# Performance work log

Measured on AMD Instinct MI355X. Metric: run time of the kernel, lower is better.

## Reference

```python
import jax, jax.numpy as jnp
import numpy as np


def setup_inputs() -> dict:
    key = jax.random.key(0)
    k1, k2 = jax.random.split(key)
    x = jax.random.normal(k1, (32, 112, 112, 64), dtype=jnp.float32)
    kernels = jax.random.normal(k2, (3, 3, 64, 128), dtype=jnp.float32) * 0.05
    biases = jnp.zeros((128,), dtype=jnp.float32)
    return {"x": x, "kernels": kernels, "biases": biases}


def reference(x, kernels, biases):
    # Stride-1 VALID cross-correlation, NHWC input, HWIO kernel -> NHWC output.
    # Matches the original's per-pixel sum(patch * kernel) over all input channels.
    out = jax.lax.conv_general_dilated(
        x, kernels,
        window_strides=(1, 1),
        padding="VALID",
        dimension_numbers=("NHWC", "HWIO", "NHWC"),
    )
    out = out + biases  # broadcast over (B, H_out, W_out, F)
    return jax.nn.relu(out)  # activation=relu per init_kwargs
```

## Files before the change

kernel.cpp:

```cpp
#include <hip/hip_runtime.h>
#include <hip/hip_bf16.h>

typedef __attribute__((ext_vector_type(4))) float f32x4;
typedef __attribute__((ext_vector_type(8))) short bf16x8;
typedef __attribute__((ext_vector_type(8))) unsigned short u16x8;
typedef __attribute__((ext_vector_type(4))) unsigned int u32x4;

#define HH 112
#define WW 112
#define CIN 64
#define COUT 128
#define HOUT 110
#define WOUT 110
#define MTOT 387200
#define NWG 3025
#define NXCD 8
#define XNE 25690112

__device__ __forceinline__ unsigned short f2bf(float f) {
  unsigned int x = __float_as_uint(f);
  x += 0x7fffu + ((x >> 16) & 1u);
  return (unsigned short)(x >> 16);
}

__device__ __forceinline__ unsigned int cvt2(float lo, float hi) {
  union { __hip_bfloat162 h; unsigned int u; } cv;
  cv.h = __float22bfloat162_rn(float2{lo, hi});
  return cv.u;
}

__device__ __forceinline__ void gload16(const unsigned short* g, unsigned short* l) {
  __builtin_amdgcn_global_load_lds(
      (const __attribute__((address_space(1))) void*)g,
      (__attribute__((address_space(3))) void*)l, 16, 0, 0);
}

__global__ __launch_bounds__(256)
void cvt_x_kernel(const float* __restrict__ x, unsigned short* __restrict__ xb) {
  const int t = blockIdx.x * 256 + threadIdx.x;
  const f32x4* s = (const f32x4*)x + (size_t)t * 2;
  f32x4 a = s[0], b = s[1];
  u32x4 v;
  v[0] = cvt2(a[0], a[1]); v[1] = cvt2(a[2], a[3]);
  v[2] = cvt2(b[0], b[1]); v[3] = cvt2(b[2], b[3]);
  ((u32x4*)xb)[t] = v;
}

__global__ void prepack_b_kernel(const float* __restrict__ kern,
                                 unsigned short* __restrict__ bt) {
  int idx = blockIdx.x * 256 + threadIdx.x;
  if (idx >= 9 * 8192) return;
  int tap = idx >> 13;
  int rem = idx & 8191;
  int co = rem >> 6;
  int e = rem & 63;
  int ci = ((e * 2) ^ ((co & 7) << 4)) >> 1;
  bt[idx] = f2bf(kern[(tap * 64 + ci) * COUT + co]);
}

__global__ __launch_bounds__(512, 4)
void conv_dma_kernel(const unsigned short* __restrict__ xb,
                     const unsigned short* __restrict__ bt,
                     const float* __restrict__ bias,
                     float* __restrict__ out) {
  __shared__ __align__(16) unsigned short As[3][8192];
  __shared__ __align__(16) unsigned short Bs[2][8192];

  const int tid = threadIdx.x;
  const int lane = tid & 63;
  const int wid = tid >> 6;

  const int bid = blockIdx.x;
  const int q = NWG / NXCD, r = NWG % NXCD;
  const int xcd = bid % NXCD, i8 = bid / NXCD;
  const int wg = (xcd < r ? xcd * (q + 1) : r * (q + 1) + (xcd - r) * q) + i8;
  const int m0 = wg * 128;

  int aoff[2];
  const int obase = wid * 2048 + lane * 16;
#pragma unroll
  for (int j = 0; j < 2; ++j) {
    const int o = obase + j * 1024;
    const int rr = o >> 7;
    const int sp = ((o >> 4) & 7) ^ (rr & 7);
    const int m = m0 + rr;
    const int wo = m % WOUT;
    const int t1 = m / WOUT;
    const int ho = t1 % HOUT;
    const int bb = t1 / HOUT;
    aoff[j] = (((bb * HH) + ho) * WW + wo) * CIN + sp * 8;
  }
  const int ldsw0 = wid * 1024;
  const int ldsw1 = wid * 1024 + 512;
  const int blin0 = ldsw0 + lane * 8;
  const int blin1 = ldsw1 + lane * 8;

  const int wm = wid >> 1;
  const int wn = wid & 1;
  const int l16 = lane & 15;
  const int lk = lane >> 4;
  const int swzR = (l16 & 7) << 4;

  const int aroff0 = (wm * 32 + 0 + l16) * 64;
  const int aroff1 = (wm * 32 + 16 + l16) * 64;
  const int broff0 = (wn * 64 + 0 + l16) * 64;
  const int broff1 = (wn * 64 + 16 + l16) * 64;
  const int broff2 = (wn * 64 + 32 + l16) * 64;
  const int broff3 = (wn * 64 + 48 + l16) * 64;

  f32x4 acc[2][4];
#pragma unroll
  for (int i = 0; i < 2; ++i)
#pragma unroll
    for (int j = 0; j < 4; ++j)
      acc[i][j] = (f32x4){0.f, 0.f, 0.f, 0.f};

  auto tapoff = [](int tap) {
    const int kh = tap / 3;
    const int kw = tap - kh * 3;
    return (kh * WW + kw) * CIN;
  };

  gload16(bt + blin0, &Bs[0][ldsw0]);
  gload16(bt + blin1, &Bs[0][ldsw1]);
  gload16(xb + aoff[0], &As[0][ldsw0]);
  gload16(xb + aoff[1], &As[0][ldsw1]);
  {
    const int te = tapoff(1);
    gload16(xb + aoff[0] + te, &As[1][ldsw0]);
    gload16(xb + aoff[1] + te, &As[1][ldsw1]);
  }

#pragma unroll
  for (int kk = 0; kk < 9; ++kk) {
    if (kk < 8) {
      asm volatile("s_waitcnt vmcnt(2)" ::: "memory");
    } else {
      asm volatile("s_waitcnt vmcnt(0)" ::: "memory");
    }
    __builtin_amdgcn_s_barrier();

    if (kk < 8) {
      const int tb = (kk + 1) * 8192;
      unsigned short* bd = Bs[(kk + 1) & 1];
      gload16(bt + tb + blin0, bd + ldsw0);
      gload16(bt + tb + blin1, bd + ldsw1);
    }
    if (kk < 7) {
      const int te = tapoff(kk + 2);
      unsigned short* ad = As[(kk + 2) % 3];
      gload16(xb + aoff[0] + te, ad + ldsw0);
      gload16(xb + aoff[1] + te, ad + ldsw1);
    }

    const unsigned short* Ac = As[kk % 3];
    const unsigned short* Bc = Bs[kk & 1];
#pragma unroll
    for (int ks = 0; ks < 2; ++ks) {
      const int cbs = ((ks * 64 + lk * 16) ^ swzR) >> 1;
      bf16x8 a0 = *(const bf16x8*)(Ac + aroff0 + cbs);
      bf16x8 a1 = *(const bf16x8*)(Ac + aroff1 + cbs);
      bf16x8 b0 = *(const bf16x8*)(Bc + broff0 + cbs);
      bf16x8 b1 = *(const bf16x8*)(Bc + broff1 + cbs);
      bf16x8 b2 = *(const bf16x8*)(Bc + broff2 + cbs);
      bf16x8 b3 = *(const bf16x8*)(Bc + broff3 + cbs);
      acc[0][0] = __builtin_amdgcn_mfma_f32_16x16x32_bf16(a0, b0, acc[0][0], 0, 0, 0);
      acc[0][1] = __builtin_amdgcn_mfma_f32_16x16x32_bf16(a0, b1, acc[0][1], 0, 0, 0);
      acc[0][2] = __builtin_amdgcn_mfma_f32_16x16x32_bf16(a0, b2, acc[0][2], 0, 0, 0);
      acc[0][3] = __builtin_amdgcn_mfma_f32_16x16x32_bf16(a0, b3, acc[0][3], 0, 0, 0);
      acc[1][0] = __builtin_amdgcn_mfma_f32_16x16x32_bf16(a1, b0, acc[1][0], 0, 0, 0);
      acc[1][1] = __builtin_amdgcn_mfma_f32_16x16x32_bf16(a1, b1, acc[1][1], 0, 0, 0);
      acc[1][2] = __builtin_amdgcn_mfma_f32_16x16x32_bf16(a1, b2, acc[1][2], 0, 0, 0);
      acc[1][3] = __builtin_amdgcn_mfma_f32_16x16x32_bf16(a1, b3, acc[1][3], 0, 0, 0);
    }
  }

  const int ncol = wn * 64 + l16;
  const float bv0 = bias[ncol + 0];
  const float bv1 = bias[ncol + 16];
  const float bv2 = bias[ncol + 32];
  const float bv3 = bias[ncol + 48];
  const int mrow0 = m0 + wm * 32 + lk * 4;
#pragma unroll
  for (int mf = 0; mf < 2; ++mf) {
#pragma unroll
    for (int j = 0; j < 4; ++j) {
      const int row = mrow0 + mf * 16 + j;
      float* orow = out + (size_t)row * COUT + ncol;
      orow[0]  = fmaxf(acc[mf][0][j] + bv0, 0.f);
      orow[16] = fmaxf(acc[mf][1][j] + bv1, 0.f);
      orow[32] = fmaxf(acc[mf][2][j] + bv2, 0.f);
      orow[48] = fmaxf(acc[mf][3][j] + bv3, 0.f);
    }
  }
}

__global__ __launch_bounds__(512)
void conv_fallback_kernel(const float* __restrict__ x,
                          const float* __restrict__ kern,
                          const float* __restrict__ bias,
                          float* __restrict__ out) {
  __shared__ __align__(16) unsigned short As[2][128 * 64];
  __shared__ __align__(16) unsigned short Bs[2][128 * 64];

  const int tid = threadIdx.x;
  const int m0 = blockIdx.x * 128;

  const int sr = tid >> 2;
  const int sc = tid & 3;
  const int m = m0 + sr;
  const int wo = m % WOUT;
  const int t1 = m / WOUT;
  const int ho = t1 % HOUT;
  const int b = t1 / HOUT;
  const float* xrow = x + (((b * HH) + ho) * WW + wo) * CIN + sc * 16;
  const int swzS = (sr & 7) << 4;
  const int awoff0 = sr * 64 + ((((sc * 32) + 0) ^ swzS) >> 1);
  const int awoff1 = sr * 64 + ((((sc * 32) + 16) ^ swzS) >> 1);

  const int bci = tid >> 3;
  const int bco = (tid & 7) * 16;

  const int lane = tid & 63;
  const int wid = tid >> 6;
  const int wm = wid >> 1;
  const int wn = wid & 1;
  const int l16 = lane & 15;
  const int lk = lane >> 4;
  const int swzR = (l16 & 7) << 4;

  const int aroff0 = (wm * 32 + 0 + l16) * 64;
  const int aroff1 = (wm * 32 + 16 + l16) * 64;
  const int broff0 = (wn * 64 + 0 + l16) * 64;
  const int broff1 = (wn * 64 + 16 + l16) * 64;
  const int broff2 = (wn * 64 + 32 + l16) * 64;
  const int broff3 = (wn * 64 + 48 + l16) * 64;

  f32x4 acc[2][4];
#pragma unroll
  for (int i = 0; i < 2; ++i)
#pragma unroll
    for (int j = 0; j < 4; ++j)
      acc[i][j] = (f32x4){0.f, 0.f, 0.f, 0.f};

  {
    f32x4 f0 = *(const f32x4*)(xrow + 0);
    f32x4 f1 = *(const f32x4*)(xrow + 4);
    f32x4 f2 = *(const f32x4*)(xrow + 8);
    f32x4 f3 = *(const f32x4*)(xrow + 12);
    u32x4 va, vb;
    va[0] = cvt2(f0[0], f0[1]); va[1] = cvt2(f0[2], f0[3]);
    va[2] = cvt2(f1[0], f1[1]); va[3] = cvt2(f1[2], f1[3]);
    vb[0] = cvt2(f2[0], f2[1]); vb[1] = cvt2(f2[2], f2[3]);
    vb[2] = cvt2(f3[0], f3[1]); vb[3] = cvt2(f3[2], f3[3]);
    *(u32x4*)(As[0] + awoff0) = va;
    *(u32x4*)(As[0] + awoff1) = vb;
    const float* kslab = kern + bci * COUT + bco;
    f32x4 g0 = *(const f32x4*)(kslab + 0);
    f32x4 g1 = *(const f32x4*)(kslab + 4);
    f32x4 g2 = *(const f32x4*)(kslab + 8);
    f32x4 g3 = *(const f32x4*)(kslab + 12);
#pragma unroll
    for (int j = 0; j < 4; ++j) {
      int c0 = bco + j;
      Bs[0][c0 * 64 + (((bci * 2) ^ ((c0 & 7) << 4)) >> 1)] = f2bf(g0[j]);
      int c1 = bco + 4 + j;
      Bs[0][c1 * 64 + (((bci * 2) ^ ((c1 & 7) << 4)) >> 1)] = f2bf(g1[j]);
      int c2 = bco + 8 + j;
      Bs[0][c2 * 64 + (((bci * 2) ^ ((c2 & 7) << 4)) >> 1)] = f2bf(g2[j]);
      int c3 = bco + 12 + j;
      Bs[0][c3 * 64 + (((bci * 2) ^ ((c3 & 7) << 4)) >> 1)] = f2bf(g3[j]);
    }
  }

#pragma unroll
  for (int kk = 0; kk < 9; ++kk) {
    const int cur = kk & 1;
    const int nxt = cur ^ 1;

    f32x4 g0, g1, g2, g3;
    f32x4 h0, h1, h2, h3;
    if (kk < 8) {
      const int kn = kk + 1;
      const int kh2 = kn / 3;
      const int kw2 = kn - kh2 * 3;
      const float* src = xrow + (kh2 * WW + kw2) * CIN;
      g0 = *(const f32x4*)(src + 0);
      g1 = *(const f32x4*)(src + 4);
      g2 = *(const f32x4*)(src + 8);
      g3 = *(const f32x4*)(src + 12);
      const float* kslab = kern + (kn * 64 + bci) * COUT + bco;
      h0 = *(const f32x4*)(kslab + 0);
      h1 = *(const f32x4*)(kslab + 4);
      h2 = *(const f32x4*)(kslab + 8);
      h3 = *(const f32x4*)(kslab + 12);
    }

    __syncthreads();

    const unsigned short* Ac = As[cur];
    const unsigned short* Bc = Bs[cur];
#pragma unroll
    for (int ks = 0; ks < 2; ++ks) {
      const int cbs = ((ks * 64 + lk * 16) ^ swzR) >> 1;
      bf16x8 a0 = *(const bf16x8*)(Ac + aroff0 + cbs);
      bf16x8 a1 = *(const bf16x8*)(Ac + aroff1 + cbs);
      bf16x8 b0 = *(const bf16x8*)(Bc + broff0 + cbs);
      bf16x8 b1 = *(const bf16x8*)(Bc + broff1 + cbs);
      bf16x8 b2 = *(const bf16x8*)(Bc + broff2 + cbs);
      bf16x8 b3 = *(const bf16x8*)(Bc + broff3 + cbs);
      acc[0][0] = __builtin_amdgcn_mfma_f32_16x16x32_bf16(a0, b0, acc[0][0], 0, 0, 0);
      acc[0][1] = __builtin_amdgcn_mfma_f32_16x16x32_bf16(a0, b1, acc[0][1], 0, 0, 0);
      acc[0][2] = __builtin_amdgcn_mfma_f32_16x16x32_bf16(a0, b2, acc[0][2], 0, 0, 0);
      acc[0][3] = __builtin_amdgcn_mfma_f32_16x16x32_bf16(a0, b3, acc[0][3], 0, 0, 0);
      acc[1][0] = __builtin_amdgcn_mfma_f32_16x16x32_bf16(a1, b0, acc[1][0], 0, 0, 0);
      acc[1][1] = __builtin_amdgcn_mfma_f32_16x16x32_bf16(a1, b1, acc[1][1], 0, 0, 0);
      acc[1][2] = __builtin_amdgcn_mfma_f32_16x16x32_bf16(a1, b2, acc[1][2], 0, 0, 0);
      acc[1][3] = __builtin_amdgcn_mfma_f32_16x16x32_bf16(a1, b3, acc[1][3], 0, 0, 0);
    }

    if (kk < 8) {
      u32x4 va, vb;
      va[0] = cvt2(g0[0], g0[1]); va[1] = cvt2(g0[2], g0[3]);
      va[2] = cvt2(g1[0], g1[1]); va[3] = cvt2(g1[2], g1[3]);
      vb[0] = cvt2(g2[0], g2[1]); vb[1] = cvt2(g2[2], g2[3]);
      vb[2] = cvt2(g3[0], g3[1]); vb[3] = cvt2(g3[2], g3[3]);
      *(u32x4*)(As[nxt] + awoff0) = va;
      *(u32x4*)(As[nxt] + awoff1) = vb;
#pragma unroll
      for (int j = 0; j < 4; ++j) {
        int c0 = bco + j;
        Bs[nxt][c0 * 64 + (((bci * 2) ^ ((c0 & 7) << 4)) >> 1)] = f2bf(h0[j]);
        int c1 = bco + 4 + j;
        Bs[nxt][c1 * 64 + (((bci * 2) ^ ((c1 & 7) << 4)) >> 1)] = f2bf(h1[j]);
        int c2 = bco + 8 + j;
        Bs[nxt][c2 * 64 + (((bci * 2) ^ ((c2 & 7) << 4)) >> 1)] = f2bf(h2[j]);
        int c3 = bco + 12 + j;
        Bs[nxt][c3 * 64 + (((bci * 2) ^ ((c3 & 7) << 4)) >> 1)] = f2bf(h3[j]);
      }
    }
  }

  const int ncol = wn * 64 + l16;
  const float bv0 = bias[ncol + 0];
  const float bv1 = bias[ncol + 16];
  const float bv2 = bias[ncol + 32];
  const float bv3 = bias[ncol + 48];
  const int mrow0 = m0 + wm * 32 + lk * 4;
#pragma unroll
  for (int mf = 0; mf < 2; ++mf) {
#pragma unroll
    for (int j = 0; j < 4; ++j) {
      const int row = mrow0 + mf * 16 + j;
      float* orow = out + (size_t)row * COUT + ncol;
      orow[0]  = fmaxf(acc[mf][0][j] + bv0, 0.f);
      orow[16] = fmaxf(acc[mf][1][j] + bv1, 0.f);
      orow[32] = fmaxf(acc[mf][2][j] + bv2, 0.f);
      orow[48] = fmaxf(acc[mf][3][j] + bv3, 0.f);
    }
  }
}

extern "C" void kernel_launch(void* const* d_in, const int* in_sizes, int n_in,
                              void* d_out, int out_size, void* d_ws, size_t ws_size,
                              hipStream_t stream) {
  const float* x = (const float*)d_in[0];
  const float* kern = (const float*)d_in[1];
  const float* bias = (const float*)d_in[2];
  float* out = (float*)d_out;

  const size_t xb_bytes = (size_t)XNE * 2;
  const size_t bt_bytes = 9 * 8192 * 2;
  if (d_ws != nullptr && ws_size >= xb_bytes + bt_bytes) {
    unsigned short* xb = (unsigned short*)d_ws;
    unsigned short* bt = xb + XNE;
    cvt_x_kernel<<<12544, 256, 0, stream>>>(x, xb);
    prepack_b_kernel<<<288, 256, 0, stream>>>(kern, bt);
    conv_dma_kernel<<<NWG, 512, 0, stream>>>(xb, bt, bias, out);
  } else {
    conv_fallback_kernel<<<3025, 512, 0, stream>>>(x, kern, bias, out);
  }
}
```

Baseline: 105.3 us.

## Fuse input bf16 conversion into conv kernel with per-output-row LDS halo tile

```diff
diff --git a/kernel.cpp b/kernel.cpp
--- a/kernel.cpp
+++ b/kernel.cpp
@@ -6,16 +6,14 @@
 typedef __attribute__((ext_vector_type(8))) unsigned short u16x8;
 typedef __attribute__((ext_vector_type(4))) unsigned int u32x4;
 
-#define HH 112
-#define WW 112
+#define IH 112
+#define IW 112
 #define CIN 64
 #define COUT 128
 #define HOUT 110
 #define WOUT 110
 #define MTOT 387200
-#define NWG 3025
-#define NXCD 8
-#define XNE 25690112
+#define NWGF 3520
 
 __device__ __forceinline__ unsigned short f2bf(float f) {
   unsigned int x = __float_as_uint(f);
@@ -33,17 +31,6 @@
   __builtin_amdgcn_global_load_lds(
       (const __attribute__((address_space(1))) void*)g,
       (__attribute__((address_space(3))) void*)l, 16, 0, 0);
-}
-
-__global__ __launch_bounds__(256)
-void cvt_x_kernel(const float* __restrict__ x, unsigned short* __restrict__ xb) {
-  const int t = blockIdx.x * 256 + threadIdx.x;
-  const f32x4* s = (const f32x4*)x + (size_t)t * 2;
-  f32x4 a = s[0], b = s[1];
-  u32x4 v;
-  v[0] = cvt2(a[0], a[1]); v[1] = cvt2(a[2], a[3]);
-  v[2] = cvt2(b[0], b[1]); v[3] = cvt2(b[2], b[3]);
-  ((u32x4*)xb)[t] = v;
 }
 
 __global__ void prepack_b_kernel(const float* __restrict__ kern,
@@ -59,11 +46,11 @@
 }
 
 __global__ __launch_bounds__(512, 4)
-void conv_dma_kernel(const unsigned short* __restrict__ xb,
-                     const unsigned short* __restrict__ bt,
-                     const float* __restrict__ bias,
-                     float* __restrict__ out) {
-  __shared__ __align__(16) unsigned short As[3][8192];
+void conv_fused_kernel(const float* __restrict__ x,
+                       const unsigned short* __restrict__ bt,
+                       const float* __restrict__ bias,
+                       float* __restrict__ out) {
+  __shared__ __align__(16) unsigned short Asl[336 * 64];
   __shared__ __align__(16) unsigned short Bs[2][8192];
 
   const int tid = threadIdx.x;
@@ -71,38 +58,50 @@
   const int wid = tid >> 6;
 
   const int bid = blockIdx.x;
-  const int q = NWG / NXCD, r = NWG % NXCD;
-  const int xcd = bid % NXCD, i8 = bid / NXCD;
-  const int wg = (xcd < r ? xcd * (q + 1) : r * (q + 1) + (xcd - r) * q) + i8;
-  const int m0 = wg * 128;
-
-  int aoff[2];
-  const int obase = wid * 2048 + lane * 16;
-#pragma unroll
-  for (int j = 0; j < 2; ++j) {
-    const int o = obase + j * 1024;
-    const int rr = o >> 7;
-    const int sp = ((o >> 4) & 7) ^ (rr & 7);
-    const int m = m0 + rr;
-    const int wo = m % WOUT;
-    const int t1 = m / WOUT;
-    const int ho = t1 % HOUT;
-    const int bb = t1 / HOUT;
-    aoff[j] = (((bb * HH) + ho) * WW + wo) * CIN + sp * 8;
-  }
+  const int wg = (bid & 7) * 440 + (bid >> 3);
+  const int bb = wg / 110;
+  const int ho = wg - bb * 110;
+
   const int ldsw0 = wid * 1024;
   const int ldsw1 = wid * 1024 + 512;
   const int blin0 = ldsw0 + lane * 8;
   const int blin1 = ldsw1 + lane * 8;
 
+  gload16(bt + blin0, &Bs[0][ldsw0]);
+  gload16(bt + blin1, &Bs[0][ldsw1]);
+
+  {
+    const float* xbase = x + ((size_t)(bb * IH + ho) * IW) * CIN;
+    for (int it = tid; it < 672; it += 512) {
+      const int u = it >> 1;
+      const int h = it & 1;
+      const int kh = u / 112;
+      const int p = u - kh * 112;
+      const float* src = xbase + (kh * IW + p) * CIN + h * 32;
+      const int key = u & 7;
+      unsigned short* rowp = Asl + u * 64;
+#pragma unroll
+      for (int c2 = 0; c2 < 4; ++c2) {
+        f32x4 a = *(const f32x4*)(src + c2 * 8);
+        f32x4 b = *(const f32x4*)(src + c2 * 8 + 4);
+        u32x4 v;
+        v[0] = cvt2(a[0], a[1]); v[1] = cvt2(a[2], a[3]);
+        v[2] = cvt2(b[0], b[1]); v[3] = cvt2(b[2], b[3]);
+        const int c = h * 4 + c2;
+        *(u32x4*)(rowp + ((c ^ key) << 3)) = v;
+      }
+    }
+  }
+  __syncthreads();
+
   const int wm = wid >> 1;
   const int wn = wid & 1;
   const int l16 = lane & 15;
   const int lk = lane >> 4;
-  const int swzR = (l16 & 7) << 4;
-
-  const int aroff0 = (wm * 32 + 0 + l16) * 64;
-  const int aroff1 = (wm * 32 + 16 + l16) * 64;
+  const int swzB = (l16 & 7) << 4;
+
+  const int am0 = wm * 32 + l16;
+  const int am1 = wm * 32 + 16 + l16;
   const int broff0 = (wn * 64 + 0 + l16) * 64;
   const int broff1 = (wn * 64 + 16 + l16) * 64;
   const int broff2 = (wn * 64 + 32 + l16) * 64;
@@ -115,51 +114,31 @@
     for (int j = 0; j < 4; ++j)
       acc[i][j] = (f32x4){0.f, 0.f, 0.f, 0.f};
 
-  auto tapoff = [](int tap) {
-    const int kh = tap / 3;
-    const int kw = tap - kh * 3;
-    return (kh * WW + kw) * CIN;
-  };
-
-  gload16(bt + blin0, &Bs[0][ldsw0]);
-  gload16(bt + blin1, &Bs[0][ldsw1]);
-  gload16(xb + aoff[0], &As[0][ldsw0]);
-  gload16(xb + aoff[1], &As[0][ldsw1]);
-  {
-    const int te = tapoff(1);
-    gload16(xb + aoff[0] + te, &As[1][ldsw0]);
-    gload16(xb + aoff[1] + te, &As[1][ldsw1]);
-  }
-
 #pragma unroll
   for (int kk = 0; kk < 9; ++kk) {
-    if (kk < 8) {
-      asm volatile("s_waitcnt vmcnt(2)" ::: "memory");
-    } else {
-      asm volatile("s_waitcnt vmcnt(0)" ::: "memory");
-    }
-    __builtin_amdgcn_s_barrier();
-
     if (kk < 8) {
       const int tb = (kk + 1) * 8192;
       unsigned short* bd = Bs[(kk + 1) & 1];
       gload16(bt + tb + blin0, bd + ldsw0);
       gload16(bt + tb + blin1, bd + ldsw1);
     }
-    if (kk < 7) {
-      const int te = tapoff(kk + 2);
-      unsigned short* ad = As[(kk + 2) % 3];
-      gload16(xb + aoff[0] + te, ad + ldsw0);
-      gload16(xb + aoff[1] + te, ad + ldsw1);
-    }
-
-    const unsigned short* Ac = As[kk % 3];
+
+    const int kh = kk / 3;
+    const int kw = kk - kh * 3;
+    int p0 = am0 + kw; if (p0 > 111) p0 = 111;
+    int p1 = am1 + kw; if (p1 > 111) p1 = 111;
+    const unsigned short* ar0 = Asl + (kh * 112 + p0) * 64;
+    const unsigned short* ar1 = Asl + (kh * 112 + p1) * 64;
+    const int sz0 = (p0 & 7) << 4;
+    const int sz1 = (p1 & 7) << 4;
     const unsigned short* Bc = Bs[kk & 1];
+
 #pragma unroll
     for (int ks = 0; ks < 2; ++ks) {
-      const int cbs = ((ks * 64 + lk * 16) ^ swzR) >> 1;
-      bf16x8 a0 = *(const bf16x8*)(Ac + aroff0 + cbs);
-      bf16x8 a1 = *(const bf16x8*)(Ac + aroff1 + cbs);
+      const int kb = ks * 64 + lk * 16;
+      bf16x8 a0 = *(const bf16x8*)(ar0 + ((kb ^ sz0) >> 1));
+      bf16x8 a1 = *(const bf16x8*)(ar1 + ((kb ^ sz1) >> 1));
+      const int cbs = (kb ^ swzB) >> 1;
       bf16x8 b0 = *(const bf16x8*)(Bc + broff0 + cbs);
       bf16x8 b1 = *(const bf16x8*)(Bc + broff1 + cbs);
       bf16x8 b2 = *(const bf16x8*)(Bc + broff2 + cbs);
@@ -173,6 +152,11 @@
       acc[1][2] = __builtin_amdgcn_mfma_f32_16x16x32_bf16(a1, b2, acc[1][2], 0, 0, 0);
       acc[1][3] = __builtin_amdgcn_mfma_f32_16x16x32_bf16(a1, b3, acc[1][3], 0, 0, 0);
     }
+
+    if (kk < 8) {
+      asm volatile("s_waitcnt vmcnt(0)" ::: "memory");
+      __builtin_amdgcn_s_barrier();
+    }
   }
 
   const int ncol = wn * 64 + l16;
@@ -180,17 +164,20 @@
   const float bv1 = bias[ncol + 16];
   const float bv2 = bias[ncol + 32];
   const float bv3 = bias[ncol + 48];
-  const int mrow0 = m0 + wm * 32 + lk * 4;
+  const size_t mbase = (size_t)bb * 12100 + (size_t)ho * 110;
 #pragma unroll
   for (int mf = 0; mf < 2; ++mf) {
+    const int wo0 = wm * 32 + mf * 16 + lk * 4;
 #pragma unroll
     for (int j = 0; j < 4; ++j) {
-      const int row = mrow0 + mf * 16 + j;
-      float* orow = out + (size_t)row * COUT + ncol;
-      orow[0]  = fmaxf(acc[mf][0][j] + bv0, 0.f);
-      orow[16] = fmaxf(acc[mf][1][j] + bv1, 0.f);
-      orow[32] = fmaxf(acc[mf][2][j] + bv2, 0.f);
-      orow[48] = fmaxf(acc[mf][3][j] + bv3, 0.f);
+      const int wo = wo0 + j;
+      if (wo < 110) {
+        float* orow = out + (mbase + wo) * COUT + ncol;
+        orow[0]  = fmaxf(acc[mf][0][j] + bv0, 0.f);
+        orow[16] = fmaxf(acc[mf][1][j] + bv1, 0.f);
+        orow[32] = fmaxf(acc[mf][2][j] + bv2, 0.f);
+        orow[48] = fmaxf(acc[mf][3][j] + bv3, 0.f);
+      }
     }
   }
 }
@@ -213,7 +200,7 @@
   const int t1 = m / WOUT;
   const int ho = t1 % HOUT;
   const int b = t1 / HOUT;
-  const float* xrow = x + (((b * HH) + ho) * WW + wo) * CIN + sc * 16;
+  const float* xrow = x + (((b * IH) + ho) * IW + wo) * CIN + sc * 16;
   const int swzS = (sr & 7) << 4;
   const int awoff0 = sr * 64 + ((((sc * 32) + 0) ^ swzS) >> 1);
   const int awoff1 = sr * 64 + ((((sc * 32) + 16) ^ swzS) >> 1);
@@ -284,7 +271,7 @@
       const int kn = kk + 1;
       const int kh2 = kn / 3;
       const int kw2 = kn - kh2 * 3;
-      const float* src = xrow + (kh2 * WW + kw2) * CIN;
+      const float* src = xrow + (kh2 * IW + kw2) * CIN;
       g0 = *(const f32x4*)(src + 0);
       g1 = *(const f32x4*)(src + 4);
       g2 = *(const f32x4*)(src + 8);
@@ -369,14 +356,11 @@
   const float* bias = (const float*)d_in[2];
   float* out = (float*)d_out;
 
-  const size_t xb_bytes = (size_t)XNE * 2;
   const size_t bt_bytes = 9 * 8192 * 2;
-  if (d_ws != nullptr && ws_size >= xb_bytes + bt_bytes) {
-    unsigned short* xb = (unsigned short*)d_ws;
-    unsigned short* bt = xb + XNE;
-    cvt_x_kernel<<<12544, 256, 0, stream>>>(x, xb);
+  if (d_ws != nullptr && ws_size >= bt_bytes) {
+    unsigned short* bt = (unsigned short*)d_ws;
     prepack_b_kernel<<<288, 256, 0, stream>>>(kern, bt);
-    conv_dma_kernel<<<NWG, 512, 0, stream>>>(xb, bt, bias, out);
+    conv_fused_kernel<<<NWGF, 512, 0, stream>>>(x, bt, bias, out);
   } else {
     conv_fallback_kernel<<<3025, 512, 0, stream>>>(x, kern, bias, out);
   }
```

New measurement: 111.7 us. 1.06x slower.
